# Performance work log

Hardware: AMD Instinct MI355X
Metric: run time of the kernel (lower is better)

The kernel has to match this reference:

```python
import jax, jax.numpy as jnp
import numpy as np

N = 8192       # tokens = batch x seq
D = 2048       # d_model
H = 2048       # per-expert hidden size
E = 8          # num_experts
TOP_K = 2


def setup_inputs() -> dict:
    key = jax.random.key(0)
    ks = jax.random.split(key, 6)
    x = jax.random.normal(ks[0], (N, D), dtype=jnp.float32)
    expert_weights = jax.random.uniform(ks[1], (N, TOP_K), dtype=jnp.float32)
    expert_indices = jax.random.randint(ks[2], (N, TOP_K), 0, E, dtype=jnp.int32)
    batch_size_per_expert = jnp.bincount(expert_indices.reshape(-1), length=E).astype(jnp.int32)
    scale = 0.02
    w1 = jax.random.normal(ks[3], (E, D, H), dtype=jnp.float32) * scale
    w2 = jax.random.normal(ks[4], (E, H, D), dtype=jnp.float32) * scale
    w3 = jax.random.normal(ks[5], (E, D, H), dtype=jnp.float32) * scale
    return {"x": x, "expert_weights": expert_weights, "expert_indices": expert_indices,
            "batch_size_per_expert": batch_size_per_expert, "w1": w1, "w2": w2, "w3": w3}


def reference(x, expert_weights, expert_indices, batch_size_per_expert, w1, w2, w3):
    """Math-equivalent to ParallelMLP.forward_once (non-EP path):
    sort tokens by expert, run per-expert SwiGLU MLP, unpermute and combine
    with top-k routing weights. Output does not depend on the sort order,
    so we express it as: out[t] = sum_k w[t,k] * expert_{idx[t,k]}(x[t]).
    """
    n, d = x.shape
    e = w1.shape[0]
    # Dense combine weights (n, E): scatter top-k routing weights.
    cw = jnp.zeros((n, e), x.dtype).at[jnp.arange(n)[:, None], expert_indices].add(expert_weights)
    out = jnp.zeros_like(x)
    for i in range(e):  # small fixed expert count
        h = jax.nn.silu(x @ w1[i]) * (x @ w3[i])  # (n, H) SwiGLU
        out = out + cw[:, i:i + 1] * (h @ w2[i])
    return out
```

## Files before the change

kernel.cpp:

```cpp
#include <hip/hip_runtime.h>
#include <stdint.h>

typedef unsigned short u16;
typedef __attribute__((ext_vector_type(8))) short s16x8;
typedef __attribute__((ext_vector_type(8))) unsigned short u16x8;
typedef __attribute__((ext_vector_type(4))) float f32x4;

#define N_TOK 8192
#define DDIM 2048
#define HDIM 2048
#define NROWS 16384
#define PADROWS 17408
#define MAXTILES 136
#define KTILES 64

#define W1T_OFF    0ull
#define W3T_OFF    67108864ull
#define W2T_OFF    134217728ull
#define XBF_OFF    201326592ull
#define HS_OFF     234881024ull
#define ROWTOK_OFF 303038464ull
#define POS_OFF    303108096ull
#define META_OFF   303173632ull
#define RES_OFF    0ull
#define WS_NEED    303173760ull

__device__ __forceinline__ u16 f2bf(float f) {
  union { float f; unsigned u; } v; v.f = f;
  unsigned r = v.u + 0x7fffu + ((v.u >> 16) & 1u);
  return (u16)(r >> 16);
}
__device__ __forceinline__ float bf2f(u16 u) {
  union { unsigned u; float f; } v; v.u = ((unsigned)u) << 16; return v.f;
}
__device__ __forceinline__ void gload_lds16(const u16* g, u16* l) {
  __builtin_amdgcn_global_load_lds(
      (const __attribute__((address_space(1))) unsigned int*)g,
      (__attribute__((address_space(3))) unsigned int*)l, 16, 0, 0);
}

__global__ void r1_kernel(const int* __restrict__ bsz, int* __restrict__ meta,
                          int* __restrict__ rowtok) {
  if (threadIdx.x == 0) {
    int off = 0, tbv = 0;
    meta[8] = 0; meta[17] = 0;
    for (int e = 0; e < 8; ++e) {
      meta[e] = 0;
      int c = bsz[e];
      off += c;  meta[9 + e] = off;
      tbv += (c + 127) >> 7; meta[18 + e] = tbv;
    }
  }
  for (int p = NROWS + (int)threadIdx.x; p < PADROWS; p += 256) rowtok[p] = 0;
}

__global__ void r2_kernel(const int* __restrict__ eidx, int* __restrict__ meta,
                          int* __restrict__ rowtok, int* __restrict__ posOf) {
  int i = blockIdx.x * 256 + threadIdx.x;
  int e = eidx[i];
  int p = atomicAdd(&meta[e], 1);
  int row = meta[8 + e] + p;
  rowtok[row] = i >> 1;
  posOf[i] = row;
}

__global__ void convert_x_kernel(const float* __restrict__ x, u16* __restrict__ xbf) {
  long long c = blockIdx.x * 256 + threadIdx.x;
  const float4 v0 = *(const float4*)&x[c * 8];
  const float4 v1 = *(const float4*)&x[c * 8 + 4];
  u16x8 u;
  u[0] = f2bf(v0.x); u[1] = f2bf(v0.y); u[2] = f2bf(v0.z); u[3] = f2bf(v0.w);
  u[4] = f2bf(v1.x); u[5] = f2bf(v1.y); u[6] = f2bf(v1.z); u[7] = f2bf(v1.w);
  *(u16x8*)&xbf[c * 8] = u;
}

__global__ __launch_bounds__(256) void transpose_cvt_kernel(
    const float* __restrict__ w1, const float* __restrict__ w2, const float* __restrict__ w3,
    u16* __restrict__ w1T, u16* __restrict__ w2T, u16* __restrict__ w3T) {
  __shared__ float tile[64][65];
  int z = blockIdx.z;
  const float* src; u16* dst;
  if (z < 8)        { src = w1 + (size_t)z * 4194304;        dst = w1T + (size_t)z * 4194304; }
  else if (z < 16)  { src = w3 + (size_t)(z - 8) * 4194304;  dst = w3T + (size_t)(z - 8) * 4194304; }
  else              { src = w2 + (size_t)(z - 16) * 4194304; dst = w2T + (size_t)(z - 16) * 4194304; }
  int r0 = blockIdx.y * 64, c0 = blockIdx.x * 64;
  int tid = threadIdx.x;
  int lr = tid >> 4, lc4 = (tid & 15) * 4;
#pragma unroll
  for (int i = 0; i < 4; ++i) {
    const float4 v = *(const float4*)&src[(size_t)(r0 + lr + i * 16) * 2048 + c0 + lc4];
    tile[lr + i * 16][lc4 + 0] = v.x; tile[lr + i * 16][lc4 + 1] = v.y;
    tile[lr + i * 16][lc4 + 2] = v.z; tile[lr + i * 16][lc4 + 3] = v.w;
  }
  __syncthreads();
  int orb = tid >> 3, oc8 = (tid & 7) * 8;
#pragma unroll
  for (int i = 0; i < 2; ++i) {
    int orow = orb + i * 32;
    u16x8 u;
#pragma unroll
    for (int j = 0; j < 8; ++j) u[j] = f2bf(tile[oc8 + j][orow]);
    *(u16x8*)&dst[(size_t)(c0 + orow) * 2048 + r0 + oc8] = u;
  }
}

template<int EPI>
__device__ __forceinline__ void gemm_body(
    const u16* __restrict__ A, const u16* __restrict__ B1m, const u16* __restrict__ B3m,
    const int* __restrict__ gather, const int* __restrict__ meta, u16* __restrict__ out) {
  const int* offs = meta + 8;
  const int* tb = meta + 17;

  const int NCOLB = EPI ? 32 : 16;
  const int CG = NCOLB / 4;
  const int nper = (MAXTILES * NCOLB) / 8;
  const int lin = (int)blockIdx.x;
  const int w = (lin & 7) * nper + (lin >> 3);
  const int sb = w >> 5, t5 = w & 31;
  const int tileId = (sb / CG) * 8 + (t5 >> 2);
  const int colb = (sb % CG) * 4 + (t5 & 3);

  if (tileId >= tb[8]) return;
  int e = 0;
#pragma unroll
  for (int qq = 1; qq < 8; ++qq) if (tileId >= tb[qq]) e = qq;
  const int row0 = offs[e] + (tileId - tb[e]) * 128;
  const int vr = offs[e + 1] - row0;

  const int bRowA = EPI ? colb * 64 : colb * 128;
  const int bRowB = EPI ? colb * 64 : colb * 128 + 64;

  __shared__ u16 lds[2][8192];

  const int tid = threadIdx.x;
  const int wid = tid >> 6, lane = tid & 63;
  const int lm = lane & 15, kg = lane >> 4;
  const int wr = wid >> 1, wc = wid & 1;

  const u16* pA[2]; const u16* pB1; const u16* pB3;
  int dA[2], dB1, dB3;
#pragma unroll
  for (int l = 0; l < 2; ++l) {
    int S = (wid + l * 4) * 64 + lane;
    int r = S >> 2;
    int c8 = ((S & 3) ^ ((r >> 1) & 3)) * 8;
    int ga = row0 + r;
    int ta = gather ? gather[ga] : ga;
    pA[l] = A + (size_t)ta * 2048 + c8;
    dA[l] = (wid + l * 4) * 512;
  }
  {
    int S = wid * 64 + lane;
    int r = S >> 2;
    int c8 = ((S & 3) ^ ((r >> 1) & 3)) * 8;
    pB1 = B1m + ((size_t)e * 2048 + bRowA + r) * 2048 + c8;
    pB3 = B3m + ((size_t)e * 2048 + bRowB + r) * 2048 + c8;
    dB1 = 4096 + wid * 512;
    dB3 = 6144 + wid * 512;
  }

  const int fK = (kg ^ ((lm >> 1) & 3)) * 8;
  const int aBase  = (wr * 64 + lm) * 32 + fK;
  const int b1Base = 4096 + (wc * 32 + lm) * 32 + fK;

  f32x4 acc1[4][2], acc3[4][2];
  f32x4 z4 = {0.f, 0.f, 0.f, 0.f};
#pragma unroll
  for (int m = 0; m < 4; ++m)
#pragma unroll
    for (int n = 0; n < 2; ++n) { acc1[m][n] = z4; acc3[m][n] = z4; }

  s16x8 a[4], b1[2], b3[2];

#define STG_ALL(bf) do { \
    gload_lds16(pA[0], &lds[bf][dA[0]]); \
    gload_lds16(pA[1], &lds[bf][dA[1]]); \
    gload_lds16(pB1,   &lds[bf][dB1]); \
    gload_lds16(pB3,   &lds[bf][dB3]); \
    pA[0] += 32; pA[1] += 32; pB1 += 32; pB3 += 32; } while (0)
#define READS(cur) do { \
_Pragma("unroll") \
    for (int mi = 0; mi < 4; ++mi) \
      a[mi] = *(const s16x8*)&lds[cur][aBase + mi * 512]; \
_Pragma("unroll") \
    for (int n = 0; n < 2; ++n) { \
      b1[n] = *(const s16x8*)&lds[cur][b1Base + n * 512]; \
      b3[n] = *(const s16x8*)&lds[cur][b1Base + 2048 + n * 512]; \
    } } while (0)
#define MFMA16() do { \
    __builtin_amdgcn_s_setprio(1); \
_Pragma("unroll") \
    for (int mi = 0; mi < 4; ++mi) \
_Pragma("unroll") \
      for (int n = 0; n < 2; ++n) { \
        acc1[mi][n] = __builtin_amdgcn_mfma_f32_16x16x32_bf16(a[mi], b1[n], acc1[mi][n], 0, 0, 0); \
        acc3[mi][n] = __builtin_amdgcn_mfma_f32_16x16x32_bf16(a[mi], b3[n], acc3[mi][n], 0, 0, 0); \
      } \
    __builtin_amdgcn_s_setprio(0); } while (0)

#define TILE_MAIN(cur) do { \
    STG_ALL(cur ^ 1); \
    asm volatile("s_waitcnt vmcnt(4)" ::: "memory"); \
    __builtin_amdgcn_s_barrier(); \
    READS(cur); \
    __builtin_amdgcn_s_barrier(); \
    MFMA16(); } while (0)
#define TILE_LAST(cur) do { \
    asm volatile("s_waitcnt vmcnt(0)" ::: "memory"); \
    __builtin_amdgcn_s_barrier(); \
    READS(cur); \
    MFMA16(); } while (0)

  STG_ALL(0);

  for (int t = 0; t < KTILES - 2; t += 2) {
    TILE_MAIN(0);
    TILE_MAIN(1);
  }
  TILE_MAIN(0);
  TILE_LAST(1);

#pragma unroll
  for (int m = 0; m < 4; ++m)
#pragma unroll
    for (int n = 0; n < 2; ++n) {
      const int rloc = wr * 64 + m * 16 + kg * 4;
      if (EPI == 1) {
        const int col = colb * 64 + wc * 32 + n * 16 + lm;
#pragma unroll
        for (int rr = 0; rr < 4; ++rr) {
          int rowl = rloc + rr;
          if (rowl < vr) {
            float z = acc1[m][n][rr];
            float h = z / (1.f + __expf(-z)) * acc3[m][n][rr];
            out[(size_t)(row0 + rowl) * 2048 + col] = f2bf(h);
          }
        }
      } else {
        const int col = colb * 128 + wc * 32 + n * 16 + lm;
#pragma unroll
        for (int rr = 0; rr < 4; ++rr) {
          int rowl = rloc + rr;
          if (rowl < vr) {
            out[(size_t)(row0 + rowl) * 2048 + col] = f2bf(acc1[m][n][rr]);
            out[(size_t)(row0 + rowl) * 2048 + col + 64] = f2bf(acc3[m][n][rr]);
          }
        }
      }
    }
#undef STG_ALL
#undef READS
#undef MFMA16
#undef TILE_MAIN
#undef TILE_LAST
}

__global__ __launch_bounds__(256, 3) void gemm1_kernel(
    const u16* __restrict__ A, const u16* __restrict__ B1m, const u16* __restrict__ B3m,
    const int* __restrict__ gather, const int* __restrict__ meta, u16* __restrict__ out) {
  gemm_body<1>(A, B1m, B3m, gather, meta, out);
}
__global__ __launch_bounds__(256, 3) void gemm2_kernel(
    const u16* __restrict__ A, const u16* __restrict__ B1m, const u16* __restrict__ B3m,
    const int* __restrict__ gather, const int* __restrict__ meta, u16* __restrict__ out) {
  gemm_body<0>(A, B1m, B3m, gather, meta, out);
}

__global__ void combine_kernel(const u16* __restrict__ res, const int* __restrict__ posOf,
                               const float* __restrict__ ew, float* __restrict__ out) {
  int c = blockIdx.x * 256 + threadIdx.x;
  int t = c >> 8, dc = (c & 255) * 8;
  int p0 = posOf[2 * t], p1 = posOf[2 * t + 1];
  float wa = ew[2 * t], wb = ew[2 * t + 1];
  u16x8 u0 = *(const u16x8*)&res[(size_t)p0 * 2048 + dc];
  u16x8 u1 = *(const u16x8*)&res[(size_t)p1 * 2048 + dc];
  float4 o0, o1;
  o0.x = wa * bf2f(u0[0]) + wb * bf2f(u1[0]);
  o0.y = wa * bf2f(u0[1]) + wb * bf2f(u1[1]);
  o0.z = wa * bf2f(u0[2]) + wb * bf2f(u1[2]);
  o0.w = wa * bf2f(u0[3]) + wb * bf2f(u1[3]);
  o1.x = wa * bf2f(u0[4]) + wb * bf2f(u1[4]);
  o1.y = wa * bf2f(u0[5]) + wb * bf2f(u1[5]);
  o1.z = wa * bf2f(u0[6]) + wb * bf2f(u1[6]);
  o1.w = wa * bf2f(u0[7]) + wb * bf2f(u1[7]);
  *(float4*)&out[(size_t)t * 2048 + dc] = o0;
  *(float4*)&out[(size_t)t * 2048 + dc + 4] = o1;
}

extern "C" void kernel_launch(void* const* d_in, const int* in_sizes, int n_in,
                              void* d_out, int out_size, void* d_ws, size_t ws_size,
                              hipStream_t stream) {
  const float* x  = (const float*)d_in[0];
  const float* ew = (const float*)d_in[1];
  const int* eidx = (const int*)d_in[2];
  const int* bsz  = (const int*)d_in[3];
  const float* w1 = (const float*)d_in[4];
  const float* w2 = (const float*)d_in[5];
  const float* w3 = (const float*)d_in[6];
  float* out = (float*)d_out;
  char* ws = (char*)d_ws;

  if (ws_size < WS_NEED) {
    hipMemsetAsync(d_out, 0, (size_t)out_size * 4, stream);
    return;
  }

  u16* w1T = (u16*)(ws + W1T_OFF);
  u16* w3T = (u16*)(ws + W3T_OFF);
  u16* w2T = (u16*)(ws + W2T_OFF);
  u16* xbf = (u16*)(ws + XBF_OFF);
  u16* hs  = (u16*)(ws + HS_OFF);
  u16* res = (u16*)(ws + RES_OFF);
  int* rowtok = (int*)(ws + ROWTOK_OFF);
  int* posOf  = (int*)(ws + POS_OFF);
  int* meta   = (int*)(ws + META_OFF);

  r1_kernel<<<1, 256, 0, stream>>>(bsz, meta, rowtok);
  r2_kernel<<<64, 256, 0, stream>>>(eidx, meta, rowtok, posOf);
  convert_x_kernel<<<8192, 256, 0, stream>>>(x, xbf);
  transpose_cvt_kernel<<<dim3(32, 32, 24), 256, 0, stream>>>(w1, w2, w3, w1T, w2T, w3T);
  gemm1_kernel<<<MAXTILES * 32, 256, 0, stream>>>(xbf, w1T, w3T, rowtok, meta, hs);
  gemm2_kernel<<<MAXTILES * 16, 256, 0, stream>>>(hs, w2T, w2T, nullptr, meta, res);
  combine_kernel<<<8192, 256, 0, stream>>>(res, posOf, ew, out);
}
```

Before: 748.9 us.

## Split GEMM K-tile into two half-phases interleaving LDS reads, loads, and MFMA

Restructures the double-buffered GEMM main loop so each K-tile runs in two phases. Phase one reads A and B1 from LDS, issues the next A prefetch, and runs the B1 MFMAs. Phase two reads B3, issues the next B prefetch, and runs the B3 MFMAs, with finer-grained vmcnt/lgkmcnt waits and raw s_barrier plus sched_barrier fences. The aim is to overlap global-to-LDS traffic and LDS reads with MFMA work and to cut the register live range so launch bounds can rise from 3 to 4 blocks per CU. It adds more barriers per tile and risks register spills or hazards from the hand-tuned waitcnt values.

```diff
diff --git a/kernel.cpp b/kernel.cpp
--- a/kernel.cpp
+++ b/kernel.cpp
@@ -172,46 +172,68 @@
 
   s16x8 a[4], b1[2], b3[2];
 
-#define STG_ALL(bf) do { \
+#define STG_A(bf) do { \
     gload_lds16(pA[0], &lds[bf][dA[0]]); \
     gload_lds16(pA[1], &lds[bf][dA[1]]); \
-    gload_lds16(pB1,   &lds[bf][dB1]); \
-    gload_lds16(pB3,   &lds[bf][dB3]); \
-    pA[0] += 32; pA[1] += 32; pB1 += 32; pB3 += 32; } while (0)
-#define READS(cur) do { \
+    pA[0] += 32; pA[1] += 32; } while (0)
+#define STG_B(bf) do { \
+    gload_lds16(pB1, &lds[bf][dB1]); \
+    gload_lds16(pB3, &lds[bf][dB3]); \
+    pB1 += 32; pB3 += 32; } while (0)
+#define READ_A4(cur) do { \
 _Pragma("unroll") \
     for (int mi = 0; mi < 4; ++mi) \
-      a[mi] = *(const s16x8*)&lds[cur][aBase + mi * 512]; \
-_Pragma("unroll") \
-    for (int n = 0; n < 2; ++n) { \
-      b1[n] = *(const s16x8*)&lds[cur][b1Base + n * 512]; \
-      b3[n] = *(const s16x8*)&lds[cur][b1Base + 2048 + n * 512]; \
-    } } while (0)
-#define MFMA16() do { \
+      a[mi] = *(const s16x8*)&lds[cur][aBase + mi * 512]; } while (0)
+#define READ_B1(cur) do { \
+_Pragma("unroll") \
+    for (int n = 0; n < 2; ++n) \
+      b1[n] = *(const s16x8*)&lds[cur][b1Base + n * 512]; } while (0)
+#define READ_B3(cur) do { \
+_Pragma("unroll") \
+    for (int n = 0; n < 2; ++n) \
+      b3[n] = *(const s16x8*)&lds[cur][b1Base + 2048 + n * 512]; } while (0)
+#define MFMA8(ACC, B) do { \
     __builtin_amdgcn_s_setprio(1); \
 _Pragma("unroll") \
     for (int mi = 0; mi < 4; ++mi) \
 _Pragma("unroll") \
-      for (int n = 0; n < 2; ++n) { \
-        acc1[mi][n] = __builtin_amdgcn_mfma_f32_16x16x32_bf16(a[mi], b1[n], acc1[mi][n], 0, 0, 0); \
-        acc3[mi][n] = __builtin_amdgcn_mfma_f32_16x16x32_bf16(a[mi], b3[n], acc3[mi][n], 0, 0, 0); \
-      } \
+      for (int n = 0; n < 2; ++n) \
+        ACC[mi][n] = __builtin_amdgcn_mfma_f32_16x16x32_bf16(a[mi], B[n], ACC[mi][n], 0, 0, 0); \
     __builtin_amdgcn_s_setprio(0); } while (0)
+#define ABAR() asm volatile("s_barrier" ::: "memory")
+#define LGKM0_FENCE() do { asm volatile("s_waitcnt lgkmcnt(0)" ::: "memory"); \
+    __builtin_amdgcn_sched_barrier(0); } while (0)
 
 #define TILE_MAIN(cur) do { \
-    STG_ALL(cur ^ 1); \
-    asm volatile("s_waitcnt vmcnt(4)" ::: "memory"); \
-    __builtin_amdgcn_s_barrier(); \
-    READS(cur); \
-    __builtin_amdgcn_s_barrier(); \
-    MFMA16(); } while (0)
+     \
+    READ_A4(cur); READ_B1(cur); \
+    STG_A(cur ^ 1); \
+    asm volatile("s_waitcnt vmcnt(2) lgkmcnt(4)" ::: "memory"); \
+    ABAR(); LGKM0_FENCE(); \
+    MFMA8(acc1, b1); \
+    ABAR(); \
+     \
+    READ_B3(cur); \
+    STG_B(cur ^ 1); \
+    asm volatile("s_waitcnt vmcnt(1)" ::: "memory"); \
+    ABAR(); LGKM0_FENCE(); \
+    MFMA8(acc3, b3); \
+    ABAR(); } while (0)
+
 #define TILE_LAST(cur) do { \
-    asm volatile("s_waitcnt vmcnt(0)" ::: "memory"); \
-    __builtin_amdgcn_s_barrier(); \
-    READS(cur); \
-    MFMA16(); } while (0)
-
-  STG_ALL(0);
+    READ_A4(cur); READ_B1(cur); \
+    asm volatile("s_waitcnt vmcnt(0) lgkmcnt(4)" ::: "memory"); \
+    ABAR(); LGKM0_FENCE(); \
+    MFMA8(acc1, b1); \
+    ABAR(); \
+    READ_B3(cur); \
+    LGKM0_FENCE(); \
+    MFMA8(acc3, b3); } while (0)
+
+  STG_A(0);
+  STG_B(0);
+  asm volatile("s_waitcnt vmcnt(1)" ::: "memory");
+  ABAR();
 
   for (int t = 0; t < KTILES - 2; t += 2) {
     TILE_MAIN(0);
@@ -248,19 +270,24 @@
         }
       }
     }
-#undef STG_ALL
-#undef READS
-#undef MFMA16
+#undef STG_A
+#undef STG_B
+#undef READ_A4
+#undef READ_B1
+#undef READ_B3
+#undef MFMA8
+#undef ABAR
+#undef LGKM0_FENCE
 #undef TILE_MAIN
 #undef TILE_LAST
 }
 
-__global__ __launch_bounds__(256, 3) void gemm1_kernel(
+__global__ __launch_bounds__(256, 4) void gemm1_kernel(
     const u16* __restrict__ A, const u16* __restrict__ B1m, const u16* __restrict__ B3m,
     const int* __restrict__ gather, const int* __restrict__ meta, u16* __restrict__ out) {
   gemm_body<1>(A, B1m, B3m, gather, meta, out);
 }
-__global__ __launch_bounds__(256, 3) void gemm2_kernel(
+__global__ __launch_bounds__(256, 4) void gemm2_kernel(
     const u16* __restrict__ A, const u16* __restrict__ B1m, const u16* __restrict__ B3m,
     const int* __restrict__ gather, const int* __restrict__ meta, u16* __restrict__ out) {
   gemm_body<0>(A, B1m, B3m, gather, meta, out);
```

Result: no change. 747.1 us (-0.2%).
